# Performance work log

Hardware: AMD Instinct MI355X
Metric: run time of the kernel (lower is better)

The kernel has to match this reference:

```python
import jax, jax.numpy as jnp
import numpy as np


def setup_inputs() -> dict:
    key = jax.random.key(0)
    ks = jax.random.split(key, 5)
    B, Cin, Cout, H, W, L, K = 16, 512, 512, 64, 64, 512, 3
    return {
        "content": jax.random.normal(ks[0], (B, Cin, H, W), jnp.float32),
        "latent": jax.random.normal(ks[1], (B, L), jnp.float32),
        "noise": jax.random.normal(ks[2], (B, 1, H, W), jnp.float32),
        "affine_w": jax.random.normal(ks[3], (Cin, L), jnp.float32),
        "affine_b": jnp.ones((Cin,), jnp.float32),  # ConvLayer fills affine bias with 1
        "conv_w": jax.random.normal(ks[4], (Cout, Cin, K, K), jnp.float32),
        "bias": jnp.zeros((1, Cout, 1, 1), jnp.float32),
        "noise_weight": jnp.asarray(0.1, jnp.float32),  # nonzero so noise path is exercised
    }


def reference(content, latent, noise, affine_w, affine_b, conv_w, bias, noise_weight):
    L = affine_w.shape[1]
    # affine (LinearLayer, lrelu=False): weight scaled by sqrt(1/inChannels), lrMultiplier=1
    style = latent @ (affine_w * np.sqrt(1.0 / L)).T + affine_b  # [B, Cin]
    # modulate: per-sample weights [B, Cout, Cin, k, k]
    w = conv_w[None] * style[:, None, :, None, None]
    # demodulate
    norm = jax.lax.rsqrt(jnp.sum(jnp.square(w), axis=(2, 3, 4), keepdims=True) + 1e-8)
    w = w * norm
    pad = conv_w.shape[-1] // 2
    # groups=batch trick == per-sample conv; vmap over batch
    def conv1(x, wk):  # x: [Cin,H,W], wk: [Cout,Cin,k,k]
        return jax.lax.conv_general_dilated(x[None], wk, (1, 1), [(pad, pad), (pad, pad)])[0]
    out = jax.vmap(conv1)(content, w)  # [B, Cout, H, W]
    out = out + noise_weight * noise
    out = jax.nn.leaky_relu(out + bias, negative_slope=0.2) * np.sqrt(2.0)
    return out
```

## Files before the change

### kernel.cpp

```cpp
#include <hip/hip_runtime.h>
#include <hip/hip_bf16.h>


typedef float f32x4 __attribute__((ext_vector_type(4)));
typedef short bf16x8 __attribute__((ext_vector_type(8)));
typedef int i32x4 __attribute__((ext_vector_type(4)));

#define BB 16
#define CIN 512
#define COUT 512
#define HH 64
#define WW 64
#define LL 512

#define XS_OFF 0
#define XS_SZ (BB * HH * WW * CIN * 2)
#define WT_OFF (XS_OFF + XS_SZ)
#define WT_SZ (9 * COUT * CIN * 2)
#define STYLE_OFF (WT_OFF + WT_SZ)
#define STYLE_SZ (BB * CIN * 4)
#define WSQ_OFF (STYLE_OFF + STYLE_SZ)
#define WSQ_SZ (COUT * CIN * 4)
#define DEM_OFF (WSQ_OFF + WSQ_SZ)
#define DEM_SZ (BB * COUT * 4)
#define WS_NEEDED (DEM_OFF + DEM_SZ)

#define XS_STRIDE 66
#define XROWB (XS_STRIDE * 64)
#define XROWS 10
#define XSZ (XROWS * XROWB)
#define WTAPB (64 * 64)
#define WSZ (9 * WTAPB)
#define LDSZ (XSZ + WSZ)

__device__ __forceinline__ void gld_lds16(const void* g, void* l) {
  __builtin_amdgcn_global_load_lds(
      (const __attribute__((address_space(1))) unsigned int*)g,
      (__attribute__((address_space(3))) unsigned int*)l, 16, 0, 0);
}

__global__ void style_kernel(const float* __restrict__ latent,
                             const float* __restrict__ affine_w,
                             const float* __restrict__ affine_b,
                             float* __restrict__ style) {
  const int idx = blockIdx.x * 256 + threadIdx.x;
  const int b = idx >> 9, ci = idx & 511;
  const float* lp = latent + b * LL;
  const float* wp = affine_w + ci * LL;
  float acc = 0.f;
  for (int l = 0; l < LL; ++l) acc += lp[l] * wp[l];
  style[idx] = acc * 0.044194173824159216f + affine_b[ci];
}

__global__ void wprep_kernel(const float* __restrict__ conv_w,
                             float* __restrict__ wsq,
                             __hip_bfloat16* __restrict__ wt) {
  const int idx = blockIdx.x * 256 + threadIdx.x;
  const int co = idx >> 9, ci = idx & 511;
  const float* wp = conv_w + idx * 9;
  float ss = 0.f;
#pragma unroll
  for (int t = 0; t < 9; ++t) {
    float v = wp[t];
    ss += v * v;
    wt[(t * COUT + co) * CIN + ci] = __float2bfloat16(v);
  }
  wsq[idx] = ss;
}

__global__ void dem_kernel(const float* __restrict__ wsq,
                           const float* __restrict__ style,
                           float* __restrict__ dem) {
  const int idx = blockIdx.x * 256 + threadIdx.x;
  const int b = idx >> 9, co = idx & 511;
  const float* sp = style + b * CIN;
  const float* wp = wsq + co * CIN;
  float acc = 0.f;
  for (int ci = 0; ci < CIN; ++ci) {
    float s = sp[ci];
    acc += wp[ci] * s * s;
  }
  dem[idx] = 1.0f / sqrtf(acc + 1e-8f);
}

__global__ void xsprep_kernel(const float* __restrict__ content,
                              const float* __restrict__ style,
                              __hip_bfloat16* __restrict__ xs) {
  __shared__ float tile[64][65];
  const int b = blockIdx.x >> 6;
  const int y = blockIdx.x & 63;
  const int tid = threadIdx.x;
  for (int cb = 0; cb < 8; ++cb) {
    const int ci0 = cb * 64;
    {
      const int x = tid & 63;
      const int c0 = tid >> 6;
#pragma unroll
      for (int p = 0; p < 16; ++p) {
        const int ci = p * 4 + c0;
        tile[ci][x] = content[((b * CIN + ci0 + ci) * HH + y) * WW + x];
      }
    }
    __syncthreads();
    {
      const int ci = tid & 63;
      const int x0 = tid >> 6;
      const float st = style[b * CIN + ci0 + ci];
#pragma unroll
      for (int p = 0; p < 16; ++p) {
        const int x = p * 4 + x0;
        xs[((b * HH + y) * WW + x) * CIN + ci0 + ci] =
            __float2bfloat16(tile[ci][x] * st);
      }
    }
    __syncthreads();
  }
}

__global__ __launch_bounds__(256, 2) void conv_kernel(
    const __hip_bfloat16* __restrict__ xs,
    const __hip_bfloat16* __restrict__ wt,
    const float* __restrict__ dem,
    const float* __restrict__ noise,
    const float* __restrict__ biasp,
    const float* __restrict__ nwp,
    float* __restrict__ out) {
  __shared__ __attribute__((aligned(16))) char lds[LDSZ];

  const int tid = threadIdx.x;
  const int lane = tid & 63;
  const int wv = tid >> 6;

  const int d = blockIdx.x;
  const int L = (d & 7) * 128 + (d >> 3);
  const int cot = L & 7;
  const int yo = (L >> 3) & 7;
  const int b = L >> 6;
  const int co0 = cot << 6;
  const int y0 = yo << 3;

  for (int off = tid * 16; off < XSZ; off += 256 * 16)
    *(i32x4*)(lds + off) = (i32x4){0, 0, 0, 0};

  const int l15 = lane & 15;
  const int kg = lane >> 4;

  int aoff[4];
#pragma unroll
  for (int mf = 0; mf < 4; ++mf) {
    const int co_l = l15 + mf * 16;
    const int fs = (co_l & 3) ^ ((co_l >> 2) & 3);
    aoff[mf] = co_l * 64 + ((kg ^ fs) << 4);
  }
  int boff[4][3];
#pragma unroll
  for (int q = 0; q < 4; ++q)
#pragma unroll
    for (int dx = 0; dx < 3; ++dx) {
      const int s = q * 16 + l15 + dx;
      const int fs = (s & 3) ^ ((s >> 2) & 3);
      boff[q][dx] = s * 64 + ((kg ^ fs) << 4);
    }

  const int rlo = (yo == 0) ? 1 : 0;
  const int rhi = (yo == 7) ? 8 : 9;
  const int nxc = (rhi - rlo + 1) * 4;
  const int ntot = nxc + 36;

  const int xsub = lane >> 2;
  const int slotl = lane & 3;

  f32x4 acc[4][8];
#pragma unroll
  for (int mf = 0; mf < 4; ++mf)
#pragma unroll
    for (int nf = 0; nf < 8; ++nf) acc[mf][nf] = (f32x4){0.f, 0.f, 0.f, 0.f};

  __syncthreads();

  for (int cib = 0; cib < 16; ++cib) {
    const int ci0 = cib * 32;
    for (int c = wv; c < ntot; c += 4) {
      if (c < nxc) {
        const int r = rlo + (c >> 2);
        const int q = c & 3;
        const int s = 1 + q * 16 + xsub;
        const int x = s - 1;
        const int y = y0 + r - 1;
        const int dcig = slotl ^ ((s & 3) ^ ((s >> 2) & 3));
        const __hip_bfloat16* g =
            xs + (((b << 6) + y) << 6 | x) * CIN + ci0 + dcig * 8;
        gld_lds16(g, lds + r * XROWB + 64 + q * 1024);
      } else {
        const int cw = c - nxc;
        const int tap = cw >> 2;
        const int q = cw & 3;
        const int co = q * 16 + xsub;
        const int dcig = slotl ^ ((co & 3) ^ ((co >> 2) & 3));
        const __hip_bfloat16* g =
            wt + ((tap << 9) + co0 + co) * CIN + ci0 + dcig * 8;
        gld_lds16(g, lds + XSZ + tap * WTAPB + q * 1024);
      }
    }
    __syncthreads();

    const int rowbase = (2 * wv) * XROWB;
#pragma unroll
    for (int dx = 0; dx < 3; ++dx) {
      bf16x8 a[3][4];
#pragma unroll
      for (int dy = 0; dy < 3; ++dy)
#pragma unroll
        for (int mf = 0; mf < 4; ++mf)
          a[dy][mf] =
              *(const bf16x8*)(lds + XSZ + (dy * 3 + dx) * WTAPB + aoff[mf]);
#pragma unroll
      for (int ir = 0; ir < 4; ++ir) {
        const char* rp = lds + rowbase + ir * XROWB;
        bf16x8 bq[4];
#pragma unroll
        for (int q = 0; q < 4; ++q)
          bq[q] = *(const bf16x8*)(rp + boff[q][dx]);
#pragma unroll
        for (int dy = 0; dy < 3; ++dy) {
          const int r = ir - dy;
          if (r == 0 || r == 1) {
#pragma unroll
            for (int q = 0; q < 4; ++q)
#pragma unroll
              for (int mf = 0; mf < 4; ++mf)
                acc[mf][r * 4 + q] = __builtin_amdgcn_mfma_f32_16x16x32_bf16(
                    a[dy][mf], bq[q], acc[mf][r * 4 + q], 0, 0, 0);
          }
        }
      }
    }
    __syncthreads();
  }

  const float nwv = nwp[0];
#pragma unroll
  for (int r = 0; r < 2; ++r) {
    const int y = y0 + 2 * wv + r;
    float nz[4];
#pragma unroll
    for (int q = 0; q < 4; ++q)
      nz[q] = nwv * noise[(b << 12) + (y << 6) + q * 16 + l15];

#pragma unroll
    for (int mf = 0; mf < 4; ++mf) {
      const int cobase = co0 + mf * 16 + kg * 4;
      const f32x4 dm = *(const f32x4*)(dem + (b << 9) + cobase);
      const f32x4 bs = *(const f32x4*)(biasp + cobase);
#pragma unroll
      for (int r2 = 0; r2 < 4; ++r2) {
        const int co = cobase + r2;
        float* op = out + ((((b << 9) + co) << 12) | (y << 6) | l15);
        const float dmv = dm[r2];
        const float bsv = bs[r2];
#pragma unroll
        for (int q = 0; q < 4; ++q) {
          float v = acc[mf][r * 4 + q][r2] * dmv + nz[q] + bsv;
          v = (v > 0.f ? v : 0.2f * v) * 1.41421356237309515f;
          op[q * 16] = v;
        }
      }
    }
  }
}

extern "C" void kernel_launch(void* const* d_in, const int* in_sizes, int n_in,
                              void* d_out, int out_size, void* d_ws, size_t ws_size,
                              hipStream_t stream) {
  const float* content  = (const float*)d_in[0];
  const float* latent   = (const float*)d_in[1];
  const float* noise    = (const float*)d_in[2];
  const float* affine_w = (const float*)d_in[3];
  const float* affine_b = (const float*)d_in[4];
  const float* conv_w   = (const float*)d_in[5];
  const float* bias     = (const float*)d_in[6];
  const float* nw       = (const float*)d_in[7];
  float* out = (float*)d_out;
  char* ws = (char*)d_ws;

  if (ws_size < (size_t)WS_NEEDED) return;

  __hip_bfloat16* xs = (__hip_bfloat16*)(ws + XS_OFF);
  __hip_bfloat16* wt = (__hip_bfloat16*)(ws + WT_OFF);
  float* style = (float*)(ws + STYLE_OFF);
  float* wsq   = (float*)(ws + WSQ_OFF);
  float* dem   = (float*)(ws + DEM_OFF);

  style_kernel<<<dim3(32), dim3(256), 0, stream>>>(latent, affine_w, affine_b, style);
  wprep_kernel<<<dim3(1024), dim3(256), 0, stream>>>(conv_w, wsq, wt);
  dem_kernel<<<dim3(32), dim3(256), 0, stream>>>(wsq, style, dem);
  xsprep_kernel<<<dim3(1024), dim3(256), 0, stream>>>(content, style, xs);
  conv_kernel<<<dim3(1024), dim3(256), 0, stream>>>(xs, wt, dem, noise, bias, nw, out);
}
```

Before: 313.2 us.

## Load conv weight fragments directly from global in MFMA-ready layout, bypassing LDS

The weight-prep kernel now writes bf16 weights pre-swizzled into per-lane MFMA A-fragment order, so the conv kernel reads A operands straight from global memory (through L1/L2) instead of staging all 9 taps through LDS each ci-block. This frees LDS (only the input tile remains), which may allow higher occupancy, and removes the weight global-to-LDS copies. The block-index remap that grouped blocks by cout tile is also dropped in favour of a linear mapping. The risk is extra global load latency inside the MFMA loop and cache pressure, since four waves each reload the same fragments.

```diff
diff --git a/kernel.cpp b/kernel.cpp
--- a/kernel.cpp
+++ b/kernel.cpp
@@ -29,9 +29,7 @@
 #define XROWB (XS_STRIDE * 64)
 #define XROWS 10
 #define XSZ (XROWS * XROWB)
-#define WTAPB (64 * 64)
-#define WSZ (9 * WTAPB)
-#define LDSZ (XSZ + WSZ)
+#define LDSZ XSZ
 
 __device__ __forceinline__ void gld_lds16(const void* g, void* l) {
   __builtin_amdgcn_global_load_lds(
@@ -54,16 +52,18 @@
 
 __global__ void wprep_kernel(const float* __restrict__ conv_w,
                              float* __restrict__ wsq,
-                             __hip_bfloat16* __restrict__ wt) {
+                             __hip_bfloat16* __restrict__ wt2) {
   const int idx = blockIdx.x * 256 + threadIdx.x;
   const int co = idx >> 9, ci = idx & 511;
   const float* wp = conv_w + idx * 9;
+  const int c = ci >> 5, slot = (ci >> 3) & 3, j = ci & 7;
+  const int base = ((co >> 4) * 4 + slot) * 128 + (co & 15) * 8 + j;
   float ss = 0.f;
 #pragma unroll
   for (int t = 0; t < 9; ++t) {
     float v = wp[t];
     ss += v * v;
-    wt[(t * COUT + co) * CIN + ci] = __float2bfloat16(v);
+    wt2[(t * 16 + c) * 16384 + base] = __float2bfloat16(v);
   }
   wsq[idx] = ss;
 }
@@ -119,7 +119,7 @@
 
 __global__ __launch_bounds__(256, 2) void conv_kernel(
     const __hip_bfloat16* __restrict__ xs,
-    const __hip_bfloat16* __restrict__ wt,
+    const __hip_bfloat16* __restrict__ wt2,
     const float* __restrict__ dem,
     const float* __restrict__ noise,
     const float* __restrict__ biasp,
@@ -132,10 +132,9 @@
   const int wv = tid >> 6;
 
   const int d = blockIdx.x;
-  const int L = (d & 7) * 128 + (d >> 3);
-  const int cot = L & 7;
-  const int yo = (L >> 3) & 7;
-  const int b = L >> 6;
+  const int cot = d & 7;
+  const int yo = (d >> 3) & 7;
+  const int b = d >> 6;
   const int co0 = cot << 6;
   const int y0 = yo << 3;
 
@@ -145,13 +144,6 @@
   const int l15 = lane & 15;
   const int kg = lane >> 4;
 
-  int aoff[4];
-#pragma unroll
-  for (int mf = 0; mf < 4; ++mf) {
-    const int co_l = l15 + mf * 16;
-    const int fs = (co_l & 3) ^ ((co_l >> 2) & 3);
-    aoff[mf] = co_l * 64 + ((kg ^ fs) << 4);
-  }
   int boff[4][3];
 #pragma unroll
   for (int q = 0; q < 4; ++q)
@@ -162,10 +154,11 @@
       boff[q][dx] = s * 64 + ((kg ^ fs) << 4);
     }
 
+  const __hip_bfloat16* abase = wt2 + (cot * 4) * 512 + lane * 8;
+
   const int rlo = (yo == 0) ? 1 : 0;
   const int rhi = (yo == 7) ? 8 : 9;
   const int nxc = (rhi - rlo + 1) * 4;
-  const int ntot = nxc + 36;
 
   const int xsub = lane >> 2;
   const int slotl = lane & 3;
@@ -180,27 +173,16 @@
 
   for (int cib = 0; cib < 16; ++cib) {
     const int ci0 = cib * 32;
-    for (int c = wv; c < ntot; c += 4) {
-      if (c < nxc) {
-        const int r = rlo + (c >> 2);
-        const int q = c & 3;
-        const int s = 1 + q * 16 + xsub;
-        const int x = s - 1;
-        const int y = y0 + r - 1;
-        const int dcig = slotl ^ ((s & 3) ^ ((s >> 2) & 3));
-        const __hip_bfloat16* g =
-            xs + (((b << 6) + y) << 6 | x) * CIN + ci0 + dcig * 8;
-        gld_lds16(g, lds + r * XROWB + 64 + q * 1024);
-      } else {
-        const int cw = c - nxc;
-        const int tap = cw >> 2;
-        const int q = cw & 3;
-        const int co = q * 16 + xsub;
-        const int dcig = slotl ^ ((co & 3) ^ ((co >> 2) & 3));
-        const __hip_bfloat16* g =
-            wt + ((tap << 9) + co0 + co) * CIN + ci0 + dcig * 8;
-        gld_lds16(g, lds + XSZ + tap * WTAPB + q * 1024);
-      }
+    for (int c = wv; c < nxc; c += 4) {
+      const int r = rlo + (c >> 2);
+      const int q = c & 3;
+      const int s = 1 + q * 16 + xsub;
+      const int x = s - 1;
+      const int y = y0 + r - 1;
+      const int dcig = slotl ^ ((s & 3) ^ ((s >> 2) & 3));
+      const __hip_bfloat16* g =
+          xs + (((b << 6) + y) << 6 | x) * CIN + ci0 + dcig * 8;
+      gld_lds16(g, lds + r * XROWB + 64 + q * 1024);
     }
     __syncthreads();
 
@@ -212,8 +194,8 @@
       for (int dy = 0; dy < 3; ++dy)
 #pragma unroll
         for (int mf = 0; mf < 4; ++mf)
-          a[dy][mf] =
-              *(const bf16x8*)(lds + XSZ + (dy * 3 + dx) * WTAPB + aoff[mf]);
+          a[dy][mf] = *(const bf16x8*)(abase +
+              ((dy * 3 + dx) * 16 + cib) * 16384 + mf * 512);
 #pragma unroll
       for (int ir = 0; ir < 4; ++ir) {
         const char* rp = lds + rowbase + ir * XROWB;
@@ -285,15 +267,15 @@
 
   if (ws_size < (size_t)WS_NEEDED) return;
 
-  __hip_bfloat16* xs = (__hip_bfloat16*)(ws + XS_OFF);
-  __hip_bfloat16* wt = (__hip_bfloat16*)(ws + WT_OFF);
+  __hip_bfloat16* xs  = (__hip_bfloat16*)(ws + XS_OFF);
+  __hip_bfloat16* wt2 = (__hip_bfloat16*)(ws + WT_OFF);
   float* style = (float*)(ws + STYLE_OFF);
   float* wsq   = (float*)(ws + WSQ_OFF);
   float* dem   = (float*)(ws + DEM_OFF);
 
   style_kernel<<<dim3(32), dim3(256), 0, stream>>>(latent, affine_w, affine_b, style);
-  wprep_kernel<<<dim3(1024), dim3(256), 0, stream>>>(conv_w, wsq, wt);
+  wprep_kernel<<<dim3(1024), dim3(256), 0, stream>>>(conv_w, wsq, wt2);
   dem_kernel<<<dim3(32), dim3(256), 0, stream>>>(wsq, style, dem);
   xsprep_kernel<<<dim3(1024), dim3(256), 0, stream>>>(content, style, xs);
-  conv_kernel<<<dim3(1024), dim3(256), 0, stream>>>(xs, wt, dem, noise, bias, nw, out);
-}
+  conv_kernel<<<dim3(1024), dim3(256), 0, stream>>>(xs, wt2, dem, noise, bias, nw, out);
+}
```

Result: slower. 343.7 us (+9.8%).

## Read activations directly from global in padded MFMA layout, double-buffer weights in LDS

Applied to the files above, without the earlier changes.

The activation prep kernel now writes a padded, channel-octet-blocked row layout with zeroed halo columns, plus a shared zero row for out-of-range y. The conv kernel loads the B operand straight from global/L2 through precomputed row pointers instead of staging input rows into LDS. Only the weights are staged in LDS, double-buffered so the next channel block's weights load while the current one computes, and one barrier per iteration is dropped. This cuts LDS traffic and synchronisation, but the inner loop now depends on global load latency and cache reuse of the activation rows across the eight co-tiles.

```diff
diff --git a/kernel.cpp b/kernel.cpp
--- a/kernel.cpp
+++ b/kernel.cpp
@@ -13,9 +13,11 @@
 #define WW 64
 #define LL 512
 
-#define XS_OFF 0
-#define XS_SZ (BB * HH * WW * CIN * 2)
-#define WT_OFF (XS_OFF + XS_SZ)
+#define XS2ROWB 81920
+
+#define XS2_OFF 0
+#define XS2_SZ (BB * HH * XS2ROWB)
+#define WT_OFF (XS2_OFF + XS2_SZ)
 #define WT_SZ (9 * COUT * CIN * 2)
 #define STYLE_OFF (WT_OFF + WT_SZ)
 #define STYLE_SZ (BB * CIN * 4)
@@ -23,15 +25,12 @@
 #define WSQ_SZ (COUT * CIN * 4)
 #define DEM_OFF (WSQ_OFF + WSQ_SZ)
 #define DEM_SZ (BB * COUT * 4)
-#define WS_NEEDED (DEM_OFF + DEM_SZ)
-
-#define XS_STRIDE 66
-#define XROWB (XS_STRIDE * 64)
-#define XROWS 10
-#define XSZ (XROWS * XROWB)
-#define WTAPB (64 * 64)
-#define WSZ (9 * WTAPB)
-#define LDSZ (XSZ + WSZ)
+#define ZROW_OFF (DEM_OFF + DEM_SZ)
+#define ZROW_SZ XS2ROWB
+#define WS_NEEDED (ZROW_OFF + ZROW_SZ)
+
+#define WBUF 36864
+#define LDSZ (2 * WBUF)
 
 __device__ __forceinline__ void gld_lds16(const void* g, void* l) {
   __builtin_amdgcn_global_load_lds(
@@ -85,13 +84,29 @@
 
 __global__ void xsprep_kernel(const float* __restrict__ content,
                               const float* __restrict__ style,
-                              __hip_bfloat16* __restrict__ xs) {
+                              __hip_bfloat16* __restrict__ xs2,
+                              __hip_bfloat16* __restrict__ zrow) {
+  const int tid = threadIdx.x;
+  if (blockIdx.x == 1024) {
+    for (int off = tid * 16; off < XS2ROWB; off += 256 * 16)
+      *(i32x4*)((char*)zrow + off) = (i32x4){0, 0, 0, 0};
+    return;
+  }
   __shared__ float tile[64][65];
   const int b = blockIdx.x >> 6;
   const int y = blockIdx.x & 63;
-  const int tid = threadIdx.x;
+  char* row = (char*)xs2 + (size_t)((b << 6) + y) * XS2ROWB;
+
+  for (int k = 0; k < 4; ++k) {
+    const int idx = tid + k * 256;
+    const int oct = idx >> 4, s = idx & 15;
+    const int off = oct * 1280 + (s < 8 ? s * 16 : 1024 + s * 16);
+    *(i32x4*)(row + off) = (i32x4){0, 0, 0, 0};
+  }
+
   for (int cb = 0; cb < 8; ++cb) {
     const int ci0 = cb * 64;
+    __syncthreads();
     {
       const int x = tid & 63;
       const int c0 = tid >> 6;
@@ -103,29 +118,36 @@
     }
     __syncthreads();
     {
-      const int ci = tid & 63;
-      const int x0 = tid >> 6;
-      const float st = style[b * CIN + ci0 + ci];
-#pragma unroll
-      for (int p = 0; p < 16; ++p) {
-        const int x = p * 4 + x0;
-        xs[((b * HH + y) * WW + x) * CIN + ci0 + ci] =
-            __float2bfloat16(tile[ci][x] * st);
+      const int x = tid & 63;
+      const int o4 = tid >> 6;
+      const int px = x + 8;
+      const int xoff = ((px >> 4) << 8) + ((px & 15) << 4);
+#pragma unroll
+      for (int oo = 0; oo < 2; ++oo) {
+        const int oct = o4 * 2 + oo;
+        bf16x8 v;
+#pragma unroll
+        for (int j = 0; j < 8; ++j) {
+          const float st = style[b * CIN + ci0 + oct * 8 + j];
+          v[j] = __bfloat16_as_short(
+              __float2bfloat16(tile[oct * 8 + j][x] * st));
+        }
+        *(bf16x8*)(row + (ci0 / 8 + oct) * 1280 + xoff) = v;
       }
     }
-    __syncthreads();
   }
 }
 
 __global__ __launch_bounds__(256, 2) void conv_kernel(
-    const __hip_bfloat16* __restrict__ xs,
+    const __hip_bfloat16* __restrict__ xs2,
     const __hip_bfloat16* __restrict__ wt,
     const float* __restrict__ dem,
     const float* __restrict__ noise,
     const float* __restrict__ biasp,
     const float* __restrict__ nwp,
+    const __hip_bfloat16* __restrict__ zrow,
     float* __restrict__ out) {
-  __shared__ __attribute__((aligned(16))) char lds[LDSZ];
+  __shared__ __attribute__((aligned(16))) char lds[2][WBUF];
 
   const int tid = threadIdx.x;
   const int lane = tid & 63;
@@ -139,11 +161,10 @@
   const int co0 = cot << 6;
   const int y0 = yo << 3;
 
-  for (int off = tid * 16; off < XSZ; off += 256 * 16)
-    *(i32x4*)(lds + off) = (i32x4){0, 0, 0, 0};
-
   const int l15 = lane & 15;
   const int kg = lane >> 4;
+  const int xsub = lane >> 2;
+  const int slotl = lane & 3;
 
   int aoff[4];
 #pragma unroll
@@ -152,23 +173,23 @@
     const int fs = (co_l & 3) ^ ((co_l >> 2) & 3);
     aoff[mf] = co_l * 64 + ((kg ^ fs) << 4);
   }
-  int boff[4][3];
+
+  const char* rp[4];
+#pragma unroll
+  for (int ir = 0; ir < 4; ++ir) {
+    const int yg = y0 + 2 * wv - 1 + ir;
+    rp[ir] = (yg >= 0 && yg < 64)
+                 ? (const char*)xs2 + (size_t)((b << 6) + yg) * XS2ROWB
+                 : (const char*)zrow;
+  }
+  int voff[4][3];
 #pragma unroll
   for (int q = 0; q < 4; ++q)
 #pragma unroll
     for (int dx = 0; dx < 3; ++dx) {
-      const int s = q * 16 + l15 + dx;
-      const int fs = (s & 3) ^ ((s >> 2) & 3);
-      boff[q][dx] = s * 64 + ((kg ^ fs) << 4);
-    }
-
-  const int rlo = (yo == 0) ? 1 : 0;
-  const int rhi = (yo == 7) ? 8 : 9;
-  const int nxc = (rhi - rlo + 1) * 4;
-  const int ntot = nxc + 36;
-
-  const int xsub = lane >> 2;
-  const int slotl = lane & 3;
+      const int p = 7 + q * 16 + l15 + dx;
+      voff[q][dx] = kg * 1280 + ((p >> 4) << 8) + ((p & 15) << 4);
+    }
 
   f32x4 acc[4][8];
 #pragma unroll
@@ -176,35 +197,27 @@
 #pragma unroll
     for (int nf = 0; nf < 8; ++nf) acc[mf][nf] = (f32x4){0.f, 0.f, 0.f, 0.f};
 
-  __syncthreads();
-
+  auto stageW = [&](int cibs, char* wbuf) {
+    const int ci0 = cibs * 32;
+    for (int i = wv; i < 36; i += 4) {
+      const int tap = i >> 2, q = i & 3;
+      const int co = q * 16 + xsub;
+      const int dcig = slotl ^ ((co & 3) ^ ((co >> 2) & 3));
+      const __hip_bfloat16* g =
+          wt + ((tap << 9) + co0 + co) * CIN + ci0 + dcig * 8;
+      gld_lds16(g, wbuf + tap * 4096 + q * 1024);
+    }
+  };
+
+  stageW(0, lds[0]);
+
+#pragma unroll 2
   for (int cib = 0; cib < 16; ++cib) {
-    const int ci0 = cib * 32;
-    for (int c = wv; c < ntot; c += 4) {
-      if (c < nxc) {
-        const int r = rlo + (c >> 2);
-        const int q = c & 3;
-        const int s = 1 + q * 16 + xsub;
-        const int x = s - 1;
-        const int y = y0 + r - 1;
-        const int dcig = slotl ^ ((s & 3) ^ ((s >> 2) & 3));
-        const __hip_bfloat16* g =
-            xs + (((b << 6) + y) << 6 | x) * CIN + ci0 + dcig * 8;
-        gld_lds16(g, lds + r * XROWB + 64 + q * 1024);
-      } else {
-        const int cw = c - nxc;
-        const int tap = cw >> 2;
-        const int q = cw & 3;
-        const int co = q * 16 + xsub;
-        const int dcig = slotl ^ ((co & 3) ^ ((co >> 2) & 3));
-        const __hip_bfloat16* g =
-            wt + ((tap << 9) + co0 + co) * CIN + ci0 + dcig * 8;
-        gld_lds16(g, lds + XSZ + tap * WTAPB + q * 1024);
-      }
-    }
     __syncthreads();
-
-    const int rowbase = (2 * wv) * XROWB;
+    if (cib < 15) stageW(cib + 1, lds[(cib + 1) & 1]);
+    const char* wb = lds[cib & 1];
+    const int cshift = cib * 5120;
+
 #pragma unroll
     for (int dx = 0; dx < 3; ++dx) {
       bf16x8 a[3][4];
@@ -212,15 +225,14 @@
       for (int dy = 0; dy < 3; ++dy)
 #pragma unroll
         for (int mf = 0; mf < 4; ++mf)
-          a[dy][mf] =
-              *(const bf16x8*)(lds + XSZ + (dy * 3 + dx) * WTAPB + aoff[mf]);
+          a[dy][mf] = *(const bf16x8*)(wb + (dy * 3 + dx) * 4096 + aoff[mf]);
 #pragma unroll
       for (int ir = 0; ir < 4; ++ir) {
-        const char* rp = lds + rowbase + ir * XROWB;
+        const char* rpc = rp[ir] + cshift;
         bf16x8 bq[4];
 #pragma unroll
         for (int q = 0; q < 4; ++q)
-          bq[q] = *(const bf16x8*)(rp + boff[q][dx]);
+          bq[q] = *(const bf16x8*)(rpc + voff[q][dx]);
 #pragma unroll
         for (int dy = 0; dy < 3; ++dy) {
           const int r = ir - dy;
@@ -235,7 +247,6 @@
         }
       }
     }
-    __syncthreads();
   }
 
   const float nwv = nwp[0];
@@ -285,15 +296,16 @@
 
   if (ws_size < (size_t)WS_NEEDED) return;
 
-  __hip_bfloat16* xs = (__hip_bfloat16*)(ws + XS_OFF);
-  __hip_bfloat16* wt = (__hip_bfloat16*)(ws + WT_OFF);
+  __hip_bfloat16* xs2  = (__hip_bfloat16*)(ws + XS2_OFF);
+  __hip_bfloat16* wt   = (__hip_bfloat16*)(ws + WT_OFF);
   float* style = (float*)(ws + STYLE_OFF);
   float* wsq   = (float*)(ws + WSQ_OFF);
   float* dem   = (float*)(ws + DEM_OFF);
+  __hip_bfloat16* zrow = (__hip_bfloat16*)(ws + ZROW_OFF);
 
   style_kernel<<<dim3(32), dim3(256), 0, stream>>>(latent, affine_w, affine_b, style);
   wprep_kernel<<<dim3(1024), dim3(256), 0, stream>>>(conv_w, wsq, wt);
   dem_kernel<<<dim3(32), dim3(256), 0, stream>>>(wsq, style, dem);
-  xsprep_kernel<<<dim3(1024), dim3(256), 0, stream>>>(content, style, xs);
-  conv_kernel<<<dim3(1024), dim3(256), 0, stream>>>(xs, wt, dem, noise, bias, nw, out);
-}
+  xsprep_kernel<<<dim3(1025), dim3(256), 0, stream>>>(content, style, xs2, zrow);
+  conv_kernel<<<dim3(1024), dim3(256), 0, stream>>>(xs2, wt, dem, noise, bias, nw, zrow, out);
+}
```

Result: slower. 364.7 us (+16.5%).
